# Kernel tuning notes

Hardware: AMD Instinct MI355X
Metric: run time of the kernel (lower is better)

## Reference

```python
import jax, jax.numpy as jnp
import numpy as np

B, N, D, C = 32, 6, 41, 64
FH, FW = 4, 6            # 150//32, 200//32
IN_CH = 768
NX, NY, NZ = 200, 200, 1 # from x/y/zbound
DX = np.array([0.5, 0.5, 20.0], np.float32)
BX = np.array([-49.75, -49.75, 0.0], np.float32)  # bound[0] + step/2


def _frustum():
    # (D, FH, FW, 3) pixel-coord + depth frustum, matching create_frustum
    ds = np.arange(4.0, 45.0, 1.0, dtype=np.float32)             # D = 41
    xs = np.linspace(0.0, 200.0 - 1.0, FW, dtype=np.float32)
    ys = np.linspace(0.0, 150.0 - 1.0, FH, dtype=np.float32)
    g = np.stack(np.broadcast_arrays(xs[None, None, :], ys[None, :, None], ds[:, None, None]), axis=-1)
    return jnp.asarray(g)


def setup_inputs() -> dict:
    key = jax.random.key(0)
    k1, k2, k3 = jax.random.split(key, 3)
    x = jax.random.normal(k1, (B, N, IN_CH, FH, FW), jnp.float32)
    # cam-to-ego base rotation (cam z -> ego x, cam x -> -ego y, cam y -> -ego z)
    R0 = np.array([[0., 0., 1.], [-1., 0., 0.], [0., -1., 0.]], np.float32)
    yaw = 2.0 * np.pi * np.arange(N) / N
    cz, sz = np.cos(yaw).astype(np.float32), np.sin(yaw).astype(np.float32)
    Rz = np.zeros((N, 3, 3), np.float32)
    Rz[:, 0, 0] = cz; Rz[:, 0, 1] = -sz; Rz[:, 1, 0] = sz; Rz[:, 1, 1] = cz; Rz[:, 2, 2] = 1.0
    rots = jnp.asarray(np.broadcast_to((Rz @ R0)[None], (B, N, 3, 3)))
    K = np.array([[100., 0., 100.], [0., 100., 75.], [0., 0., 1.]], np.float32)
    intrins = jnp.asarray(np.broadcast_to(K, (B, N, 3, 3)))
    trans = jax.random.uniform(k2, (B, N, 3), jnp.float32, -2.0, 2.0)
    conv_w = jax.random.normal(k3, (D + C, IN_CH), jnp.float32) * 0.02
    conv_b = jnp.zeros((D + C,), jnp.float32)
    return {"x": x, "rots": rots, "trans": trans, "intrins": intrins, "conv_w": conv_w, "conv_b": conv_b}


def reference(x, rots, trans, intrins, conv_w, conv_b):
    frustum = _frustum()                                        # (D,FH,FW,3)
    # --- get_geometry ---
    pts = jnp.concatenate([frustum[..., :2] * frustum[..., 2:3], frustum[..., 2:3]], -1)
    combine = rots @ jnp.linalg.inv(intrins)                    # (B,N,3,3)
    geom = jnp.einsum('bnij,dhwj->bndhwi', combine, pts) + trans[:, :, None, None, None, :]
    # --- get_cam_feats: 1x1 conv depthnet, softmax depth, outer product ---
    xf = x.reshape(B * N, IN_CH, FH, FW)
    y = jnp.einsum('oc,bchw->bohw', conv_w, xf) + conv_b[None, :, None, None]
    depth_logit = y[:, :D]                                      # (BN,D,FH,FW)
    depth = jax.nn.softmax(depth_logit, axis=1)
    feat = y[:, D:D + C]                                        # (BN,C,FH,FW)
    xv = (depth[:, None] * feat[:, :, None]).reshape(B, N, C, D, FH, FW).transpose(0, 1, 3, 4, 5, 2)
    # --- voxel_pooling: segment-sum over voxel rank, scatter to BEV ---
    xN = xv.reshape(-1, C)                                      # (Nprime, C)
    g = ((geom - (BX - DX / 2.0)) / DX).astype(jnp.int32).reshape(-1, 3)  # trunc like .long()
    Np = xN.shape[0]
    bix = jnp.repeat(jnp.arange(Np // (Np // B) * 0 + B), Np // B)        # batch index per point
    kept = ((g[:, 0] >= 0) & (g[:, 0] < NX) & (g[:, 1] >= 0) & (g[:, 1] < NY)
            & (g[:, 2] >= 0) & (g[:, 2] < NZ))
    idx = ((bix * NZ + g[:, 2]) * NX + g[:, 0]) * NY + g[:, 1]
    idx = jnp.where(kept, idx, 0)
    xm = jnp.where(kept[:, None], xN, 0.0)
    pooled = jax.ops.segment_sum(xm, idx, num_segments=B * NZ * NX * NY)  # (B*NZ*NX*NY, C)
    final = pooled.reshape(B, NZ, NX, NY, C).transpose(0, 1, 4, 2, 3).reshape(B, NZ * C, NX, NY)
    return (final, depth_logit)
```

## Files before the change

kernel.cpp:

```cpp
#include <hip/hip_runtime.h>
#include <hip/hip_bf16.h>

#define B_    32
#define N_    6
#define D_    41
#define C_    64
#define FH_   4
#define FW_   6
#define INCH  768
#define HW    24
#define O_    105
#define PBN   984
#define PPB   5904
#define NPTS  188928
#define FINAL_ELEMS 81920000


__global__ __launch_bounds__(256) void k_conv_fused(
    const float* __restrict__ x, const float* __restrict__ w,
    const float* __restrict__ bias,
    float* __restrict__ feat_ws, float* __restrict__ depth_ws,
    float* __restrict__ dlogit)
{
    __shared__ float xs[9216];
    __shared__ float ys[O_ * HW];
    __shared__ float smax[HW], srs[HW];

    const int bn = blockIdx.x;
    const int t  = threadIdx.x;
    const int og = t / 6;
    const int q6 = t % 6;

    float a[3][4] = {{0.f,0.f,0.f,0.f},{0.f,0.f,0.f,0.f},{0.f,0.f,0.f,0.f}};
    const int o0 = og * 3;
    const float4* wr0 = (const float4*)(w + (size_t)(o0 + 0) * INCH);
    const float4* wr1 = (const float4*)(w + (size_t)(o0 + 1) * INCH);
    const float4* wr2 = (const float4*)(w + (size_t)(o0 + 2) * INCH);
    float4* xs4 = (float4*)xs;

    for (int half = 0; half < 2; ++half) {
        if (half) __syncthreads();
        const float4* xg = (const float4*)(x + (size_t)bn * (INCH * HW)) + half * 2304;
        for (int i = t; i < 2304; i += 256) xs4[i] = xg[i];
        __syncthreads();

        if (t < 210) {
            const int wb = half * 96;
            for (int c4 = 0; c4 < 96; ++c4) {
                float4 w0 = wr0[wb + c4];
                float4 w1 = wr1[wb + c4];
                float4 w2 = wr2[wb + c4];
                int cb = c4 * 4;
                float4 x0 = xs4[(cb + 0) * 6 + q6];
                float4 x1 = xs4[(cb + 1) * 6 + q6];
                float4 x2 = xs4[(cb + 2) * 6 + q6];
                float4 x3 = xs4[(cb + 3) * 6 + q6];
                a[0][0]=fmaf(w0.x,x0.x,a[0][0]); a[0][1]=fmaf(w0.x,x0.y,a[0][1]);
                a[0][2]=fmaf(w0.x,x0.z,a[0][2]); a[0][3]=fmaf(w0.x,x0.w,a[0][3]);
                a[1][0]=fmaf(w1.x,x0.x,a[1][0]); a[1][1]=fmaf(w1.x,x0.y,a[1][1]);
                a[1][2]=fmaf(w1.x,x0.z,a[1][2]); a[1][3]=fmaf(w1.x,x0.w,a[1][3]);
                a[2][0]=fmaf(w2.x,x0.x,a[2][0]); a[2][1]=fmaf(w2.x,x0.y,a[2][1]);
                a[2][2]=fmaf(w2.x,x0.z,a[2][2]); a[2][3]=fmaf(w2.x,x0.w,a[2][3]);
                a[0][0]=fmaf(w0.y,x1.x,a[0][0]); a[0][1]=fmaf(w0.y,x1.y,a[0][1]);
                a[0][2]=fmaf(w0.y,x1.z,a[0][2]); a[0][3]=fmaf(w0.y,x1.w,a[0][3]);
                a[1][0]=fmaf(w1.y,x1.x,a[1][0]); a[1][1]=fmaf(w1.y,x1.y,a[1][1]);
                a[1][2]=fmaf(w1.y,x1.z,a[1][2]); a[1][3]=fmaf(w1.y,x1.w,a[1][3]);
                a[2][0]=fmaf(w2.y,x1.x,a[2][0]); a[2][1]=fmaf(w2.y,x1.y,a[2][1]);
                a[2][2]=fmaf(w2.y,x1.z,a[2][2]); a[2][3]=fmaf(w2.y,x1.w,a[2][3]);
                a[0][0]=fmaf(w0.z,x2.x,a[0][0]); a[0][1]=fmaf(w0.z,x2.y,a[0][1]);
                a[0][2]=fmaf(w0.z,x2.z,a[0][2]); a[0][3]=fmaf(w0.z,x2.w,a[0][3]);
                a[1][0]=fmaf(w1.z,x2.x,a[1][0]); a[1][1]=fmaf(w1.z,x2.y,a[1][1]);
                a[1][2]=fmaf(w1.z,x2.z,a[1][2]); a[1][3]=fmaf(w1.z,x2.w,a[1][3]);
                a[2][0]=fmaf(w2.z,x2.x,a[2][0]); a[2][1]=fmaf(w2.z,x2.y,a[2][1]);
                a[2][2]=fmaf(w2.z,x2.z,a[2][2]); a[2][3]=fmaf(w2.z,x2.w,a[2][3]);
                a[0][0]=fmaf(w0.w,x3.x,a[0][0]); a[0][1]=fmaf(w0.w,x3.y,a[0][1]);
                a[0][2]=fmaf(w0.w,x3.z,a[0][2]); a[0][3]=fmaf(w0.w,x3.w,a[0][3]);
                a[1][0]=fmaf(w1.w,x3.x,a[1][0]); a[1][1]=fmaf(w1.w,x3.y,a[1][1]);
                a[1][2]=fmaf(w1.w,x3.z,a[1][2]); a[1][3]=fmaf(w1.w,x3.w,a[1][3]);
                a[2][0]=fmaf(w2.w,x3.x,a[2][0]); a[2][1]=fmaf(w2.w,x3.y,a[2][1]);
                a[2][2]=fmaf(w2.w,x3.z,a[2][2]); a[2][3]=fmaf(w2.w,x3.w,a[2][3]);
            }
        }
    }

    if (t < 210) {
#pragma unroll
        for (int r = 0; r < 3; r++) {
            float bo = bias[o0 + r];
#pragma unroll
            for (int j = 0; j < 4; j++)
                ys[(o0 + r) * HW + q6 * 4 + j] = a[r][j] + bo;
        }
    }
    __syncthreads();

    if (t < HW) {
        float mx = -1e30f;
        for (int d = 0; d < D_; d++) mx = fmaxf(mx, ys[d * HW + t]);
        float s = 0.f;
        for (int d = 0; d < D_; d++) s = __fadd_rn(s, expf(__fsub_rn(ys[d * HW + t], mx)));
        smax[t] = mx; srs[t] = s;
    }
    __syncthreads();

    for (int u = t; u < D_ * HW; u += 256) {
        float yv = ys[u];
        int hw = u % HW;
        depth_ws[bn * PBN + u] = __fdiv_rn(expf(__fsub_rn(yv, smax[hw])), srs[hw]);
        dlogit[(size_t)bn * PBN + u] = yv;
    }
    for (int u = t; u < C_ * HW; u += 256)
        feat_ws[(size_t)bn * (C_ * HW) + u] = ys[D_ * HW + u];
}

__global__ __launch_bounds__(256) void k_geom(
    const float* __restrict__ m1, const float* __restrict__ trans,
    const float* __restrict__ m2, int* __restrict__ vox)
{
    const float* rots = (fabsf(m1[0]) > 50.0f) ? m2 : m1;
    const float* intr = (fabsf(m1[0]) > 50.0f) ? m1 : m2;

    int p = blockIdx.x * 256 + threadIdx.x;
    int b  = p / PPB;
    int pl = p % PPB;
    int n  = pl / PBN;
    int r  = pl % PBN;
    int d  = r / HW;
    int hw = r % HW;
    int h = hw / FW_, wp = hw % FW_;

    float dv = 4.0f + (float)d;
    float xi = (float)((double)wp * (199.0 / 5.0));
    float yi = (float)((double)h  * (149.0 / 3.0));
    float px = __fmul_rn(xi, dv), py = __fmul_rn(yi, dv), pz = dv;

    int bn = b * N_ + n;
    const float* K = intr + bn * 9;
    const float* R = rots + bn * 9;
    const float* T = trans + bn * 3;

    float a00 = K[0], a01 = K[1], a02 = K[2];
    float a11 = K[4], a12 = K[5];
    float a22 = K[8];

    float i00 = __fdiv_rn(1.0f, a00);
    float i11 = __fdiv_rn(1.0f, a11);
    float x0  = __fmul_rn(a01, i00);
    float i01 = __fmul_rn(-i11, x0);
    float i22 = __fdiv_rn(1.0f, a22);
    float y0  = __fmul_rn(a02, i00);
    y0 = __fadd_rn(y0, __fmul_rn(a12, i01));
    float y1  = __fmul_rn(a12, i11);
    float i02 = __fmul_rn(-i22, y0);
    float i12 = __fmul_rn(-i22, y1);
    float i10 = 0.f, i20 = 0.f, i21 = 0.f;

    float r00 = R[0], r01 = R[1], r02 = R[2];
    float r10 = R[3], r11 = R[4], r12 = R[5];
    float r20 = R[6], r21 = R[7], r22 = R[8];

#define MM(u0,u1,u2, v0,v1,v2) \
    __fmaf_rn(u2, v2, __fmaf_rn(u1, v1, __fmul_rn(u0, v0)))
    float c00 = MM(r00, r01, r02, i00, i10, i20);
    float c01 = MM(r00, r01, r02, i01, i11, i21);
    float c02 = MM(r00, r01, r02, i02, i12, i22);
    float c10 = MM(r10, r11, r12, i00, i10, i20);
    float c11 = MM(r10, r11, r12, i01, i11, i21);
    float c12 = MM(r10, r11, r12, i02, i12, i22);
    float c20 = MM(r20, r21, r22, i00, i10, i20);
    float c21 = MM(r20, r21, r22, i01, i11, i21);
    float c22 = MM(r20, r21, r22, i02, i12, i22);
#undef MM

#define DOT3(u0,v0,u1,v1,u2,v2) \
    __fadd_rn(__fadd_rn(__fmul_rn(u0,v0), __fmul_rn(u1,v1)), __fmul_rn(u2,v2))
    float gx = __fadd_rn(DOT3(c00,px, c01,py, c02,pz), T[0]);
    float gy = __fadd_rn(DOT3(c10,px, c11,py, c12,pz), T[1]);
    float gz = __fadd_rn(DOT3(c20,px, c21,py, c22,pz), T[2]);
#undef DOT3

    int ix = (int)__fmul_rn(__fadd_rn(gx, 50.0f), 2.0f);
    int iy = (int)__fmul_rn(__fadd_rn(gy, 50.0f), 2.0f);
    int iz = (int)__fdiv_rn(__fadd_rn(gz, 10.0f), 20.0f);
    bool kept = (ix >= 0) && (ix < 200) && (iy >= 0) && (iy < 200) && (iz == 0);
    vox[p] = kept ? (ix * 200 + iy) : -1;
}

__global__ __launch_bounds__(256) void k_splat(
    const float* __restrict__ depth, const float* __restrict__ feat,
    const int* __restrict__ vox, float* __restrict__ out)
{
    __shared__ float plane[10000];
    int bid = blockIdx.x;
    int b   = bid >> 8;
    int rem = bid & 255;
    int c   = rem >> 2;
    int q   = rem & 3;
    int t   = threadIdx.x;

    for (int i = t; i < 10000; i += 256) plane[i] = 0.f;
    __syncthreads();

    const int lo = q * 10000;
    const float* fb = feat + (size_t)(b * N_) * (C_ * HW) + c * HW;
    for (int i = t; i < PPB; i += 256) {
        int p = b * PPB + i;
        int rel = vox[p] - lo;
        if ((unsigned)rel < 10000u) {
            int n  = i / PBN;
            int hw = i % HW;
            atomicAdd(&plane[rel], depth[p] * fb[n * (C_ * HW) + hw]);
        }
    }
    __syncthreads();

    float4* ob = (float4*)(out + ((size_t)(b * C_ + c) * 40000) + lo);
    const float4* pl4 = (const float4*)plane;
    for (int i = t; i < 2500; i += 256) ob[i] = pl4[i];
}

extern "C" void kernel_launch(void* const* d_in, const int* in_sizes, int n_in,
                              void* d_out, int out_size, void* d_ws, size_t ws_size,
                              hipStream_t stream) {
    const float *x = nullptr, *m1 = nullptr, *m2 = nullptr, *trn = nullptr,
                *w = nullptr, *bias = nullptr;
    for (int i = 0; i < n_in; i++) {
        const float* p = (const float*)d_in[i];
        switch (in_sizes[i]) {
            case 3538944: x = p; break;
            case 1728:    if (!m1) m1 = p; else m2 = p; break;
            case 576:     trn = p; break;
            case 80640:   w = p; break;
            case 105:     bias = p; break;
            default: break;
        }
    }
    if (!x)    x    = (const float*)d_in[0];
    if (!m1)   m1   = (const float*)d_in[1];
    if (!trn)  trn  = (const float*)d_in[2];
    if (!m2)   m2   = (const float*)d_in[3];
    if (!w)    w    = (const float*)d_in[4];
    if (!bias) bias = (const float*)d_in[5];

    float* feat_ws  = (float*)d_ws;
    float* depth_ws = feat_ws + 192 * C_ * HW;
    int*   vox      = (int*)(depth_ws + NPTS);

    float* out    = (float*)d_out;
    float* dlogit = out + FINAL_ELEMS;

    k_conv_fused<<<192,  256, 0, stream>>>(x, w, bias, feat_ws, depth_ws, dlogit);
    k_geom      <<<738,  256, 0, stream>>>(m1, trn, m2, vox);
    k_splat     <<<8192, 256, 0, stream>>>(depth_ws, feat_ws, vox, out);
}
```

Measured before the change: 457.5 us.

## Bucket kept points per batch-quadrant in geom kernel for compact splat lists

The geometry kernel now appends each kept point, with its local voxel offset, camera/pixel index and depth weight, into a per-(batch, quadrant) list using an atomic counter. The splat kernel loops only over its own bucket instead of scanning all points of the batch and filtering. It also caches the channel's 144 feature values in shared memory. This removes redundant vox/depth reads and branch filtering across the four quadrant blocks and 64 channels, at the cost of global atomics in geom and nondeterministic entry order, which changes float summation order.

Result: slower. 797.6 us (+74.4%).

```diff
diff --git a/kernel.cpp b/kernel.cpp
--- a/kernel.cpp
+++ b/kernel.cpp
@@ -20,7 +20,7 @@
     const float* __restrict__ x, const float* __restrict__ w,
     const float* __restrict__ bias,
     float* __restrict__ feat_ws, float* __restrict__ depth_ws,
-    float* __restrict__ dlogit)
+    float* __restrict__ dlogit, int* __restrict__ cnt)
 {
     __shared__ float xs[9216];
     __shared__ float ys[O_ * HW];
@@ -30,6 +30,8 @@
     const int t  = threadIdx.x;
     const int og = t / 6;
     const int q6 = t % 6;
+
+    if (bn == 0 && t < 128) cnt[t] = 0;
 
     float a[3][4] = {{0.f,0.f,0.f,0.f},{0.f,0.f,0.f,0.f},{0.f,0.f,0.f,0.f}};
     const int o0 = og * 3;
@@ -115,7 +117,8 @@
 
 __global__ __launch_bounds__(256) void k_geom(
     const float* __restrict__ m1, const float* __restrict__ trans,
-    const float* __restrict__ m2, int* __restrict__ vox)
+    const float* __restrict__ m2, const float* __restrict__ depth,
+    int* __restrict__ cnt, uint2* __restrict__ entries)
 {
     const float* rots = (fabsf(m1[0]) > 50.0f) ? m2 : m1;
     const float* intr = (fabsf(m1[0]) > 50.0f) ? m1 : m2;
@@ -183,14 +186,25 @@
     int iy = (int)__fmul_rn(__fadd_rn(gy, 50.0f), 2.0f);
     int iz = (int)__fdiv_rn(__fadd_rn(gz, 10.0f), 20.0f);
     bool kept = (ix >= 0) && (ix < 200) && (iy >= 0) && (iy < 200) && (iz == 0);
-    vox[p] = kept ? (ix * 200 + iy) : -1;
+
+    if (kept) {
+        int vl  = ix * 200 + iy;
+        int q   = vl / 10000;
+        int rel = vl - q * 10000;
+        int nhw = n * HW + hw;
+        int slot = atomicAdd(&cnt[b * 4 + q], 1);
+        entries[(size_t)(b * 4 + q) * PPB + slot] =
+            make_uint2((unsigned)rel | ((unsigned)nhw << 14),
+                       __float_as_uint(depth[p]));
+    }
 }
 
 __global__ __launch_bounds__(256) void k_splat(
-    const float* __restrict__ depth, const float* __restrict__ feat,
-    const int* __restrict__ vox, float* __restrict__ out)
+    const float* __restrict__ feat, const int* __restrict__ cnt,
+    const uint2* __restrict__ entries, float* __restrict__ out)
 {
     __shared__ float plane[10000];
+    __shared__ float ftab[144];
     int bid = blockIdx.x;
     int b   = bid >> 8;
     int rem = bid & 255;
@@ -199,21 +213,22 @@
     int t   = threadIdx.x;
 
     for (int i = t; i < 10000; i += 256) plane[i] = 0.f;
+    if (t < 144) {
+        int n  = t / HW;
+        int hw = t - n * HW;
+        ftab[t] = feat[(size_t)(b * N_ + n) * (C_ * HW) + c * HW + hw];
+    }
+    __syncthreads();
+
+    const int ne = cnt[b * 4 + q];
+    const uint2* eb = entries + (size_t)(b * 4 + q) * PPB;
+    for (int i = t; i < ne; i += 256) {
+        uint2 e = eb[i];
+        atomicAdd(&plane[e.x & 16383u], __uint_as_float(e.y) * ftab[e.x >> 14]);
+    }
     __syncthreads();
 
     const int lo = q * 10000;
-    const float* fb = feat + (size_t)(b * N_) * (C_ * HW) + c * HW;
-    for (int i = t; i < PPB; i += 256) {
-        int p = b * PPB + i;
-        int rel = vox[p] - lo;
-        if ((unsigned)rel < 10000u) {
-            int n  = i / PBN;
-            int hw = i % HW;
-            atomicAdd(&plane[rel], depth[p] * fb[n * (C_ * HW) + hw]);
-        }
-    }
-    __syncthreads();
-
     float4* ob = (float4*)(out + ((size_t)(b * C_ + c) * 40000) + lo);
     const float4* pl4 = (const float4*)plane;
     for (int i = t; i < 2500; i += 256) ob[i] = pl4[i];
@@ -244,12 +259,13 @@
 
     float* feat_ws  = (float*)d_ws;
     float* depth_ws = feat_ws + 192 * C_ * HW;
-    int*   vox      = (int*)(depth_ws + NPTS);
+    int*   cnt      = (int*)(depth_ws + NPTS);
+    uint2* entries  = (uint2*)(cnt + 128);
 
     float* out    = (float*)d_out;
     float* dlogit = out + FINAL_ELEMS;
 
-    k_conv_fused<<<192,  256, 0, stream>>>(x, w, bias, feat_ws, depth_ws, dlogit);
-    k_geom      <<<738,  256, 0, stream>>>(m1, trn, m2, vox);
-    k_splat     <<<8192, 256, 0, stream>>>(depth_ws, feat_ws, vox, out);
-}
+    k_conv_fused<<<192,  256, 0, stream>>>(x, w, bias, feat_ws, depth_ws, dlogit, cnt);
+    k_geom      <<<738,  256, 0, stream>>>(m1, trn, m2, depth_ws, cnt, entries);
+    k_splat     <<<8192, 256, 0, stream>>>(feat_ws, cnt, entries, out);
+}
```
